# Kernel tuning notes

Measured on AMD Instinct MI355X. Metric: run time of the kernel, lower is better.

## Reference

```python
import jax, jax.numpy as jnp
import numpy as np

N, NFEAT, NHID, NCLASS = 10000, 512, 64, 10
ALPHA = 0.2


def setup_inputs() -> dict:
    key = jax.random.key(0)
    ks = jax.random.split(key, 8)
    x = jax.random.normal(ks[0], (N, NFEAT), dtype=jnp.float32)
    adj1 = jax.random.uniform(ks[1], (N, N), dtype=jnp.float32) / N  # row-normalized-ish
    adj2 = jax.random.uniform(ks[2], (N, N), dtype=jnp.float32) / N
    # GraphConvolution params (glorot-ish scale)
    W1 = jax.random.normal(ks[3], (NFEAT, NHID), dtype=jnp.float32) * (1.0 / np.sqrt(NFEAT))
    b1 = jnp.zeros((NHID,), dtype=jnp.float32)
    W2 = jax.random.normal(ks[4], (NFEAT, NHID), dtype=jnp.float32) * (1.0 / np.sqrt(NFEAT))
    b2 = jnp.zeros((NHID,), dtype=jnp.float32)
    attn_w = jax.random.normal(ks[5], (NHID, 1), dtype=jnp.float32) * (1.0 / np.sqrt(NHID))
    cluster = jax.random.normal(ks[6], (NCLASS, NHID), dtype=jnp.float32)
    return {"x": x, "adj1": adj1, "adj2": adj2, "W1": W1, "b1": b1,
            "W2": W2, "b2": b2, "attn_w": attn_w, "cluster": cluster}


def reference(x, adj1, adj2, W1, b1, W2, b2, attn_w, cluster):
    # Two GCN branches: output = adj @ (x @ W) + b
    emb1 = adj1 @ (x @ W1) + b1  # [N, H]
    emb2 = adj2 @ (x @ W2) + b2  # [N, H]
    z = jnp.stack([emb1, emb2], axis=1)            # [N, 2, H]
    # tiny 2-way attention fusion
    w = z @ attn_w                                  # [N, 2, 1]
    beta = jax.nn.softmax(w, axis=1)                # softmax over the 2 views
    emb = jnp.sum(beta * z, axis=1)                 # [N, H]
    # DEC cluster assignment (faithful to the original, including the
    # second power and the /2, which the row-normalization cancels)
    d2 = jnp.sum((emb[:, None, :] - cluster[None, :, :]) ** 2, axis=2)  # [N, K]
    q = 1.0 / (1.0 + d2 / ALPHA)
    q = q ** ((ALPHA + 1.0) / 2.0)
    q = q ** (ALPHA + 1.0) / 2.0
    q = q / jnp.sum(q, axis=1, keepdims=True)
    return emb, q
```

## Files before the change

kernel.cpp:

```cpp
#include <hip/hip_runtime.h>
#include <math.h>

#define NROWS 10000
#define FEAT  512
#define NHID  64
#define NCLS  10
#define YT_STRIDE 10240
#define KB_PAD 320
#define NSPLIT 8
#define CHUNK 40

typedef __attribute__((ext_vector_type(8))) short short8;
typedef __attribute__((ext_vector_type(4))) float f32x4;

__device__ __forceinline__ short f2bf(float f) {
  union { float f; unsigned u; } v; v.f = f;
  unsigned r = v.u + 0x7fffu + ((v.u >> 16) & 1u);
  return (short)(r >> 16);
}

__device__ __forceinline__ float wsum64(float v) {
#pragma unroll
  for (int off = 32; off > 0; off >>= 1) v += __shfl_xor(v, off, 64);
  return v;
}

__device__ __forceinline__ void gload16(const void* g, void* l) {
  __builtin_amdgcn_global_load_lds(
      (const __attribute__((address_space(1))) unsigned int*)g,
      (__attribute__((address_space(3))) unsigned int*)l, 16, 0, 0);
}

__global__ __launch_bounds__(256) void prep_w(const float* __restrict__ W1,
                                              const float* __restrict__ W2,
                                              unsigned short* __restrict__ Wt1,
                                              unsigned short* __restrict__ Wt2) {
  int i = blockIdx.x * 256 + threadIdx.x;
  if (i >= FEAT * NHID) return;
  int k = i >> 6, h = i & 63;
  Wt1[h * FEAT + k] = (unsigned short)f2bf(W1[i]);
  Wt2[h * FEAT + k] = (unsigned short)f2bf(W2[i]);
}

__global__ __launch_bounds__(256) void gemm_xw(const float* __restrict__ x,
                                               const unsigned short* __restrict__ Wt1,
                                               const unsigned short* __restrict__ Wt2,
                                               unsigned short* __restrict__ Yt1,
                                               unsigned short* __restrict__ Yt2) {
  const int lane = threadIdx.x & 63;
  const int wave = threadIdx.x >> 6;
  const int job = blockIdx.x * 4 + wave;
  if (job >= 1250) return;
  const int br = (job >= 625) ? 1 : 0;
  const int tile = job - 625 * br;
  const unsigned short* Wt = br ? Wt2 : Wt1;
  unsigned short* Yt       = br ? Yt2 : Yt1;
  const int rowbase = tile * 16;
  const int r16 = lane & 15, g = lane >> 4, ga = g * 8;

  const float* arow = x + (size_t)(rowbase + r16) * FEAT + ga;
  const unsigned short* bp = Wt + (size_t)r16 * FEAT + ga;

  f32x4 acc[4];
#pragma unroll
  for (int t = 0; t < 4; ++t) acc[t] = (f32x4){0.f, 0.f, 0.f, 0.f};

#pragma unroll
  for (int kb = 0; kb < FEAT / 32; ++kb) {
    const int k0 = kb * 32;
    const f32x4* ap = (const f32x4*)(arow + k0);
    f32x4 a0 = ap[0], a1 = ap[1];
    short8 af;
    af[0] = f2bf(a0[0]); af[1] = f2bf(a0[1]); af[2] = f2bf(a0[2]); af[3] = f2bf(a0[3]);
    af[4] = f2bf(a1[0]); af[5] = f2bf(a1[1]); af[6] = f2bf(a1[2]); af[7] = f2bf(a1[3]);
#pragma unroll
    for (int t = 0; t < 4; ++t) {
      short8 bf = *(const short8*)(bp + (size_t)t * 16 * FEAT + k0);
      acc[t] = __builtin_amdgcn_mfma_f32_16x16x32_bf16(af, bf, acc[t], 0, 0, 0);
    }
  }
#pragma unroll
  for (int t = 0; t < 4; ++t)
#pragma unroll
    for (int rr = 0; rr < 4; ++rr)
      Yt[(size_t)(t * 16 + r16) * YT_STRIDE + (rowbase + g * 4 + rr)] =
          (unsigned short)f2bf(acc[t][rr]);
}

__global__ __launch_bounds__(256, 3) void gemm_adj(const float* __restrict__ adj1,
                                                   const float* __restrict__ adj2,
                                                   const unsigned short* __restrict__ Yt1,
                                                   const unsigned short* __restrict__ Yt2,
                                                   float* __restrict__ Ep) {
  __shared__ __attribute__((aligned(16))) float          Asm[4][2048];
  __shared__ __attribute__((aligned(16))) unsigned short Bsm[4][2048];

  const int sp = blockIdx.y;
  const int br = blockIdx.z;
  const float* adj         = br ? adj2 : adj1;
  const unsigned short* Yt = br ? Yt2 : Yt1;
  float* E = Ep + (size_t)(br * NSPLIT + sp) * NROWS * NHID;
  const int kb0 = sp * CHUNK;
  const int blockrow = blockIdx.x * 64;

  const int lane = threadIdx.x & 63;
  const int wave = threadIdx.x >> 6;

  const int l8 = lane >> 3, v = lane & 7;
  const int arow0 = wave * 16 + l8;
  const int arow1 = wave * 16 + 8 + l8;
  const int g0 = (v >> 1) ^ (arow0 & 3), g1 = (v >> 1) ^ (arow1 & 3);
  const int akoff0 = g0 * 8 + (v & 1) * 4;
  const int akoff1 = g1 * 8 + (v & 1) * 4;
  const float* abase0 = adj + (size_t)min(blockrow + arow0, NROWS - 1) * NROWS;
  const float* abase1 = adj + (size_t)min(blockrow + arow1, NROWS - 1) * NROWS;
  const int adst0 = (wave * 2 + 0) * 256 + lane * 4;
  const int adst1 = (wave * 2 + 1) * 256 + lane * 4;
  const int bj = (lane & 3) ^ (l8 & 3);
  const unsigned short* bbase =
      Yt + (size_t)(wave * 16 + (lane >> 2)) * YT_STRIDE + bj * 8;
  const int bdst = wave * 512 + lane * 8;

  const int r16 = lane & 15, g = lane >> 4;
  const int ard  = (wave * 16 + r16) * 32 + ((g ^ (r16 & 3)) * 8);
  const int bsw  = (g ^ ((r16 >> 1) & 3)) * 8;
  const int brd0 = (0 * 16 + r16) * 32 + bsw;
  const int brd1 = (1 * 16 + r16) * 32 + bsw;
  const int brd2 = (2 * 16 + r16) * 32 + bsw;
  const int brd3 = (3 * 16 + r16) * 32 + bsw;

  f32x4 acc0 = (f32x4){0.f, 0.f, 0.f, 0.f};
  f32x4 acc1 = acc0, acc2 = acc0, acc3 = acc0;

#define STAGE(T) { const int k0s = (kb0 + (T)) * 32; const int sl = (T) & 3;      \
    gload16(abase0 + min(k0s + akoff0, NROWS - 4), &Asm[sl][adst0]);              \
    gload16(abase1 + min(k0s + akoff1, NROWS - 4), &Asm[sl][adst1]);              \
    gload16(bbase + k0s, &Bsm[sl][bdst]); }

#define RC(T) { const int sl = (T) & 3;                                           \
    const f32x4* ap = (const f32x4*)&Asm[sl][ard];                                \
    f32x4 a0 = ap[0], a1 = ap[1];                                                 \
    short8 bf0 = *(const short8*)&Bsm[sl][brd0];                                  \
    short8 bf1 = *(const short8*)&Bsm[sl][brd1];                                  \
    short8 bf2 = *(const short8*)&Bsm[sl][brd2];                                  \
    short8 bf3 = *(const short8*)&Bsm[sl][brd3];                                  \
    short8 af;                                                                    \
    af[0] = f2bf(a0[0]); af[1] = f2bf(a0[1]); af[2] = f2bf(a0[2]); af[3] = f2bf(a0[3]); \
    af[4] = f2bf(a1[0]); af[5] = f2bf(a1[1]); af[6] = f2bf(a1[2]); af[7] = f2bf(a1[3]); \
    acc0 = __builtin_amdgcn_mfma_f32_16x16x32_bf16(af, bf0, acc0, 0, 0, 0);       \
    acc1 = __builtin_amdgcn_mfma_f32_16x16x32_bf16(af, bf1, acc1, 0, 0, 0);       \
    acc2 = __builtin_amdgcn_mfma_f32_16x16x32_bf16(af, bf2, acc2, 0, 0, 0);       \
    acc3 = __builtin_amdgcn_mfma_f32_16x16x32_bf16(af, bf3, acc3, 0, 0, 0); }

  STAGE(0) STAGE(1) STAGE(2) STAGE(3)

#pragma unroll 4
  for (int t = 0; t < CHUNK - 3; ++t) {
    asm volatile("s_waitcnt vmcnt(9)" ::: "memory");
    __builtin_amdgcn_sched_barrier(0);
    __builtin_amdgcn_s_barrier();
    RC(t)
    __builtin_amdgcn_s_barrier();
    if (t < CHUNK - 4) STAGE(t + 4)
  }
  asm volatile("s_waitcnt vmcnt(6)" ::: "memory");
  __builtin_amdgcn_sched_barrier(0);
  __builtin_amdgcn_s_barrier();
  RC(CHUNK - 3)
  asm volatile("s_waitcnt vmcnt(3)" ::: "memory");
  __builtin_amdgcn_sched_barrier(0);
  __builtin_amdgcn_s_barrier();
  RC(CHUNK - 2)
  asm volatile("s_waitcnt vmcnt(0)" ::: "memory");
  __builtin_amdgcn_sched_barrier(0);
  __builtin_amdgcn_s_barrier();
  RC(CHUNK - 1)
#undef STAGE
#undef RC

#pragma unroll
  for (int rr = 0; rr < 4; ++rr) {
    const int grow = blockrow + wave * 16 + g * 4 + rr;
    if (grow < NROWS) {
      float* e = E + (size_t)grow * NHID + r16;
      e[0]  = acc0[rr];
      e[16] = acc1[rr];
      e[32] = acc2[rr];
      e[48] = acc3[rr];
    }
  }
}

__global__ __launch_bounds__(256) void gemm_adj_dyn(const float* __restrict__ adj1,
                                                    const float* __restrict__ adj2,
                                                    const unsigned short* __restrict__ Yt1,
                                                    const unsigned short* __restrict__ Yt2,
                                                    float* __restrict__ Ep,
                                                    int nsplit, int chunk) {
  const int sp = blockIdx.y;
  const int br = blockIdx.z;
  const float* adj          = br ? adj2 : adj1;
  const unsigned short* Yt  = br ? Yt2 : Yt1;
  float* E = Ep + (size_t)(br * nsplit + sp) * NROWS * NHID;

  const int kb_begin = sp * chunk;
  const int kb_end   = min(kb_begin + chunk, KB_PAD);

  const int lane = threadIdx.x & 63;
  const int wave = threadIdx.x >> 6;
  const int rowbase = blockIdx.x * 64 + wave * 16;
  if (rowbase >= NROWS) return;
  const int r = lane & 15;
  const int g = lane >> 4;
  const int ga = g * 8;

  const float* arow = adj + (size_t)(rowbase + r) * NROWS;
  const size_t boff = (size_t)r * YT_STRIDE + ga;

  f32x4 acc0 = (f32x4){0.f, 0.f, 0.f, 0.f};
  f32x4 acc1 = acc0, acc2 = acc0, acc3 = acc0;

#pragma unroll 4
  for (int kb = kb_begin; kb < kb_end; ++kb) {
    const int k0 = kb * 32;
    const int kc = min(k0 + ga, 9992);
    const f32x4* ap = (const f32x4*)(arow + kc);
    f32x4 a0 = ap[0], a1 = ap[1];
    short8 af;
    af[0] = f2bf(a0[0]); af[1] = f2bf(a0[1]); af[2] = f2bf(a0[2]); af[3] = f2bf(a0[3]);
    af[4] = f2bf(a1[0]); af[5] = f2bf(a1[1]); af[6] = f2bf(a1[2]); af[7] = f2bf(a1[3]);
    short8 bf0 = *(const short8*)(Yt + boff + k0);
    short8 bf1 = *(const short8*)(Yt + boff + 16 * YT_STRIDE + k0);
    short8 bf2 = *(const short8*)(Yt + boff + 32 * YT_STRIDE + k0);
    short8 bf3 = *(const short8*)(Yt + boff + 48 * YT_STRIDE + k0);
    acc0 = __builtin_amdgcn_mfma_f32_16x16x32_bf16(af, bf0, acc0, 0, 0, 0);
    acc1 = __builtin_amdgcn_mfma_f32_16x16x32_bf16(af, bf1, acc1, 0, 0, 0);
    acc2 = __builtin_amdgcn_mfma_f32_16x16x32_bf16(af, bf2, acc2, 0, 0, 0);
    acc3 = __builtin_amdgcn_mfma_f32_16x16x32_bf16(af, bf3, acc3, 0, 0, 0);
  }

  const size_t ebase = (size_t)(rowbase + g * 4) * NHID + r;
#pragma unroll
  for (int rr = 0; rr < 4; ++rr) {
    E[ebase + (size_t)rr * NHID +  0] = acc0[rr];
    E[ebase + (size_t)rr * NHID + 16] = acc1[rr];
    E[ebase + (size_t)rr * NHID + 32] = acc2[rr];
    E[ebase + (size_t)rr * NHID + 48] = acc3[rr];
  }
}

__global__ __launch_bounds__(256) void fuse(const float* __restrict__ Ep,
                                            int nsplit,
                                            const float* __restrict__ b1,
                                            const float* __restrict__ b2,
                                            const float* __restrict__ aw,
                                            const float* __restrict__ cl,
                                            float* __restrict__ out) {
  const int lane = threadIdx.x & 63;
  const int wave = threadIdx.x >> 6;
  const int row = blockIdx.x * 4 + wave;
  if (row >= NROWS) return;

  const size_t off = (size_t)row * NHID + lane;
  const size_t bstride = (size_t)nsplit * NROWS * NHID;
  float e1 = b1[lane], e2 = b2[lane];
  for (int s = 0; s < nsplit; ++s) {
    e1 += Ep[(size_t)s * NROWS * NHID + off];
    e2 += Ep[bstride + (size_t)s * NROWS * NHID + off];
  }

  float a = aw[lane];
  float w1 = wsum64(e1 * a);
  float w2 = wsum64(e2 * a);
  float m = fmaxf(w1, w2);
  float x1 = expf(w1 - m), x2 = expf(w2 - m);
  float inv = 1.0f / (x1 + x2);
  float emb = (x1 * e1 + x2 * e2) * inv;
  out[off] = emb;

  float myq = 0.f, qs = 0.f;
#pragma unroll
  for (int c = 0; c < NCLS; ++c) {
    float d = emb - cl[c * NHID + lane];
    float s = wsum64(d * d);
    float t = exp2f(-0.72f * log2f(fmaf(5.0f, s, 1.0f)));
    qs += t;
    if (lane == c) myq = t;
  }
  if (lane < NCLS) out[(size_t)NROWS * NHID + (size_t)row * NCLS + lane] = myq / qs;
}

extern "C" void kernel_launch(void* const* d_in, const int* in_sizes, int n_in,
                              void* d_out, int out_size, void* d_ws, size_t ws_size,
                              hipStream_t stream) {
  const float* x    = (const float*)d_in[0];
  const float* adj1 = (const float*)d_in[1];
  const float* adj2 = (const float*)d_in[2];
  const float* W1   = (const float*)d_in[3];
  const float* b1   = (const float*)d_in[4];
  const float* W2   = (const float*)d_in[5];
  const float* b2   = (const float*)d_in[6];
  const float* aw   = (const float*)d_in[7];
  const float* cl   = (const float*)d_in[8];
  float* out = (float*)d_out;

  char* ws = (char*)d_ws;
  unsigned short* Yt1 = (unsigned short*)(ws + 0);
  unsigned short* Yt2 = (unsigned short*)(ws + 1310720);
  unsigned short* Wt1 = (unsigned short*)(ws + 2621440);
  unsigned short* Wt2 = (unsigned short*)(ws + 2686976);
  float* Ep           = (float*)(ws + 2752512);

  const size_t fixed = 2752512;
  const size_t per_split = 2ull * NROWS * NHID * 4ull;
  const bool static_ok = ws_size >= fixed + (size_t)NSPLIT * per_split;

  hipMemsetAsync(Yt1, 0, 2 * 1310720, stream);
  prep_w<<<dim3(128), dim3(256), 0, stream>>>(W1, W2, Wt1, Wt2);
  gemm_xw<<<dim3(313), dim3(256), 0, stream>>>(x, Wt1, Wt2, Yt1, Yt2);

  if (static_ok) {
    gemm_adj<<<dim3(157, NSPLIT, 2), dim3(256), 0, stream>>>(adj1, adj2, Yt1, Yt2, Ep);
    fuse<<<dim3(2500), dim3(256), 0, stream>>>(Ep, NSPLIT, b1, b2, aw, cl, out);
  } else {
    int nsplit = 1;
    if (ws_size > fixed + per_split) {
      size_t s = (ws_size - fixed) / per_split;
      nsplit = (int)(s < 8 ? s : 8);
      if (nsplit < 1) nsplit = 1;
    }
    const int chunk = (KB_PAD + nsplit - 1) / nsplit;
    gemm_adj_dyn<<<dim3(157, nsplit, 2), dim3(256), 0, stream>>>(adj1, adj2, Yt1, Yt2,
                                                                 Ep, nsplit, chunk);
    fuse<<<dim3(2500), dim3(256), 0, stream>>>(Ep, nsplit, b1, b2, aw, cl, out);
  }
}
```

Measured before the change: 258.8 us.

## Retile adjacency GEMM with 32-row blocks, 256-wide K tiles and swizzled Yt

Reworks the adj@Y kernel to use 32x64 output tiles split across 4 waves (2x2), K tiles of 256 with double-buffered LDS staging, and 4 K-splits instead of 8. The Yt intermediate is written with an XOR swizzle on the row index so LDS reads of B avoid bank conflicts, and the fallback kernel is updated to match. Larger per-stage transfers aim to cut barrier and issue overhead and halve the split partials read by the fuse step. In exchange, the LDS footprint (~128KB) limits occupancy to one block per CU, and the A-tile rows are now loaded twice across blocks relative to the previous 64-row tiles.

```diff
diff --git a/kernel.cpp b/kernel.cpp
--- a/kernel.cpp
+++ b/kernel.cpp
@@ -7,8 +7,9 @@
 #define NCLS  10
 #define YT_STRIDE 10240
 #define KB_PAD 320
-#define NSPLIT 8
-#define CHUNK 40
+#define TK    256
+#define NSPLIT 4
+#define TILES_PER_SPLIT 10
 
 typedef __attribute__((ext_vector_type(8))) short short8;
 typedef __attribute__((ext_vector_type(4))) float f32x4;
@@ -79,114 +80,109 @@
       acc[t] = __builtin_amdgcn_mfma_f32_16x16x32_bf16(af, bf, acc[t], 0, 0, 0);
     }
   }
+  const int sw = (r16 & 7) << 3;
 #pragma unroll
   for (int t = 0; t < 4; ++t)
 #pragma unroll
-    for (int rr = 0; rr < 4; ++rr)
-      Yt[(size_t)(t * 16 + r16) * YT_STRIDE + (rowbase + g * 4 + rr)] =
-          (unsigned short)f2bf(acc[t][rr]);
-}
-
-__global__ __launch_bounds__(256, 3) void gemm_adj(const float* __restrict__ adj1,
+    for (int rr = 0; rr < 4; ++rr) {
+      const int col = t * 16 + r16;
+      const int row = rowbase + g * 4 + rr;
+      Yt[(size_t)col * YT_STRIDE + (row ^ sw)] = (unsigned short)f2bf(acc[t][rr]);
+    }
+}
+
+__global__ __launch_bounds__(256, 1) void gemm_adj(const float* __restrict__ adj1,
                                                    const float* __restrict__ adj2,
                                                    const unsigned short* __restrict__ Yt1,
                                                    const unsigned short* __restrict__ Yt2,
                                                    float* __restrict__ Ep) {
-  __shared__ __attribute__((aligned(16))) float          Asm[4][2048];
-  __shared__ __attribute__((aligned(16))) unsigned short Bsm[4][2048];
+  __shared__ __attribute__((aligned(16))) float          Asm[2][32 * 256];
+  __shared__ __attribute__((aligned(16))) unsigned short Bsm[2][64 * 256];
 
   const int sp = blockIdx.y;
   const int br = blockIdx.z;
   const float* adj         = br ? adj2 : adj1;
   const unsigned short* Yt = br ? Yt2 : Yt1;
   float* E = Ep + (size_t)(br * NSPLIT + sp) * NROWS * NHID;
-  const int kb0 = sp * CHUNK;
-  const int blockrow = blockIdx.x * 64;
+  const int k_base = sp * (TILES_PER_SPLIT * TK);
+  const int blockrow = blockIdx.x * 32;
 
   const int lane = threadIdx.x & 63;
   const int wave = threadIdx.x >> 6;
 
-  const int l8 = lane >> 3, v = lane & 7;
-  const int arow0 = wave * 16 + l8;
-  const int arow1 = wave * 16 + 8 + l8;
-  const int g0 = (v >> 1) ^ (arow0 & 3), g1 = (v >> 1) ^ (arow1 & 3);
-  const int akoff0 = g0 * 8 + (v & 1) * 4;
-  const int akoff1 = g1 * 8 + (v & 1) * 4;
-  const float* abase0 = adj + (size_t)min(blockrow + arow0, NROWS - 1) * NROWS;
-  const float* abase1 = adj + (size_t)min(blockrow + arow1, NROWS - 1) * NROWS;
-  const int adst0 = (wave * 2 + 0) * 256 + lane * 4;
-  const int adst1 = (wave * 2 + 1) * 256 + lane * 4;
-  const int bj = (lane & 3) ^ (l8 & 3);
-  const unsigned short* bbase =
-      Yt + (size_t)(wave * 16 + (lane >> 2)) * YT_STRIDE + bj * 8;
-  const int bdst = wave * 512 + lane * 8;
-
+  const int a_el = lane * 4;
+  const int b_cl = lane >> 5;
+  const int b_el = (lane & 31) * 8;
+
+  const int wr = wave >> 1, wc = wave & 1;
   const int r16 = lane & 15, g = lane >> 4;
-  const int ard  = (wave * 16 + r16) * 32 + ((g ^ (r16 & 3)) * 8);
-  const int bsw  = (g ^ ((r16 >> 1) & 3)) * 8;
-  const int brd0 = (0 * 16 + r16) * 32 + bsw;
-  const int brd1 = (1 * 16 + r16) * 32 + bsw;
-  const int brd2 = (2 * 16 + r16) * 32 + bsw;
-  const int brd3 = (3 * 16 + r16) * 32 + bsw;
-
-  f32x4 acc0 = (f32x4){0.f, 0.f, 0.f, 0.f};
-  f32x4 acc1 = acc0, acc2 = acc0, acc3 = acc0;
-
-#define STAGE(T) { const int k0s = (kb0 + (T)) * 32; const int sl = (T) & 3;      \
-    gload16(abase0 + min(k0s + akoff0, NROWS - 4), &Asm[sl][adst0]);              \
-    gload16(abase1 + min(k0s + akoff1, NROWS - 4), &Asm[sl][adst1]);              \
-    gload16(bbase + k0s, &Bsm[sl][bdst]); }
-
-#define RC(T) { const int sl = (T) & 3;                                           \
-    const f32x4* ap = (const f32x4*)&Asm[sl][ard];                                \
-    f32x4 a0 = ap[0], a1 = ap[1];                                                 \
-    short8 bf0 = *(const short8*)&Bsm[sl][brd0];                                  \
-    short8 bf1 = *(const short8*)&Bsm[sl][brd1];                                  \
-    short8 bf2 = *(const short8*)&Bsm[sl][brd2];                                  \
-    short8 bf3 = *(const short8*)&Bsm[sl][brd3];                                  \
-    short8 af;                                                                    \
-    af[0] = f2bf(a0[0]); af[1] = f2bf(a0[1]); af[2] = f2bf(a0[2]); af[3] = f2bf(a0[3]); \
-    af[4] = f2bf(a1[0]); af[5] = f2bf(a1[1]); af[6] = f2bf(a1[2]); af[7] = f2bf(a1[3]); \
-    acc0 = __builtin_amdgcn_mfma_f32_16x16x32_bf16(af, bf0, acc0, 0, 0, 0);       \
-    acc1 = __builtin_amdgcn_mfma_f32_16x16x32_bf16(af, bf1, acc1, 0, 0, 0);       \
-    acc2 = __builtin_amdgcn_mfma_f32_16x16x32_bf16(af, bf2, acc2, 0, 0, 0);       \
-    acc3 = __builtin_amdgcn_mfma_f32_16x16x32_bf16(af, bf3, acc3, 0, 0, 0); }
-
-  STAGE(0) STAGE(1) STAGE(2) STAGE(3)
-
-#pragma unroll 4
-  for (int t = 0; t < CHUNK - 3; ++t) {
-    asm volatile("s_waitcnt vmcnt(9)" ::: "memory");
+  const int swb = (r16 & 7) << 3;
+
+  f32x4 accL = (f32x4){0.f, 0.f, 0.f, 0.f};
+  f32x4 accH = accL;
+
+  auto STAGE = [&](int tt) {
+    const int k0 = k_base + tt * TK;
+    const int bufi = tt & 1;
+#pragma unroll
+    for (int j = 0; j < 8; ++j) {
+      const int gr = blockrow + wave * 8 + j;
+      const float* src = adj + (size_t)min(gr, NROWS - 1) * NROWS
+                             + min(k0 + a_el, NROWS - 4);
+      gload16(src, &Asm[bufi][(wave * 8 + j) * 256]);
+    }
+#pragma unroll
+    for (int j = 0; j < 8; ++j) {
+      const int c0 = wave * 16 + j * 2;
+      const unsigned short* src =
+          Yt + (size_t)(c0 + b_cl) * YT_STRIDE + (k0 + b_el);
+      gload16(src, &Bsm[bufi][c0 * 256]);
+    }
+  };
+
+  auto COMPUTE = [&](int tt) {
+    const int bufi = tt & 1;
+#pragma unroll
+    for (int s = 0; s < 8; ++s) {
+      const int kx = s * 32 + g * 8;
+      const float* ap = &Asm[bufi][(wr * 16 + r16) * 256 + kx];
+      f32x4 a0 = *(const f32x4*)ap;
+      f32x4 a1 = *(const f32x4*)(ap + 4);
+      const int colL = wc * 32 + r16;
+      short8 bL = *(const short8*)&Bsm[bufi][colL * 256 + (kx ^ swb)];
+      short8 bH = *(const short8*)&Bsm[bufi][(colL + 16) * 256 + (kx ^ swb)];
+      short8 af;
+      af[0] = f2bf(a0[0]); af[1] = f2bf(a0[1]); af[2] = f2bf(a0[2]); af[3] = f2bf(a0[3]);
+      af[4] = f2bf(a1[0]); af[5] = f2bf(a1[1]); af[6] = f2bf(a1[2]); af[7] = f2bf(a1[3]);
+      accL = __builtin_amdgcn_mfma_f32_16x16x32_bf16(af, bL, accL, 0, 0, 0);
+      accH = __builtin_amdgcn_mfma_f32_16x16x32_bf16(af, bH, accH, 0, 0, 0);
+    }
+  };
+
+  STAGE(0);
+#pragma unroll 2
+  for (int t = 0; t < TILES_PER_SPLIT - 1; ++t) {
+    STAGE(t + 1);
+    asm volatile("s_waitcnt vmcnt(16)" ::: "memory");
     __builtin_amdgcn_sched_barrier(0);
     __builtin_amdgcn_s_barrier();
-    RC(t)
+    __builtin_amdgcn_sched_barrier(0);
+    COMPUTE(t);
     __builtin_amdgcn_s_barrier();
-    if (t < CHUNK - 4) STAGE(t + 4)
-  }
-  asm volatile("s_waitcnt vmcnt(6)" ::: "memory");
-  __builtin_amdgcn_sched_barrier(0);
-  __builtin_amdgcn_s_barrier();
-  RC(CHUNK - 3)
-  asm volatile("s_waitcnt vmcnt(3)" ::: "memory");
-  __builtin_amdgcn_sched_barrier(0);
-  __builtin_amdgcn_s_barrier();
-  RC(CHUNK - 2)
+  }
   asm volatile("s_waitcnt vmcnt(0)" ::: "memory");
   __builtin_amdgcn_sched_barrier(0);
   __builtin_amdgcn_s_barrier();
-  RC(CHUNK - 1)
-#undef STAGE
-#undef RC
+  __builtin_amdgcn_sched_barrier(0);
+  COMPUTE(TILES_PER_SPLIT - 1);
 
 #pragma unroll
   for (int rr = 0; rr < 4; ++rr) {
-    const int grow = blockrow + wave * 16 + g * 4 + rr;
+    const int grow = blockrow + wr * 16 + g * 4 + rr;
     if (grow < NROWS) {
-      float* e = E + (size_t)grow * NHID + r16;
-      e[0]  = acc0[rr];
-      e[16] = acc1[rr];
-      e[32] = acc2[rr];
-      e[48] = acc3[rr];
+      float* e = E + (size_t)grow * NHID + wc * 32 + r16;
+      e[0]  = accL[rr];
+      e[16] = accH[rr];
     }
   }
 }
@@ -213,9 +209,9 @@
   const int r = lane & 15;
   const int g = lane >> 4;
   const int ga = g * 8;
+  const int sw = (r & 7) << 3;
 
   const float* arow = adj + (size_t)(rowbase + r) * NROWS;
-  const size_t boff = (size_t)r * YT_STRIDE + ga;
 
   f32x4 acc0 = (f32x4){0.f, 0.f, 0.f, 0.f};
   f32x4 acc1 = acc0, acc2 = acc0, acc3 = acc0;
@@ -224,15 +220,16 @@
   for (int kb = kb_begin; kb < kb_end; ++kb) {
     const int k0 = kb * 32;
     const int kc = min(k0 + ga, 9992);
+    const int ks = (k0 + ga) ^ sw;
     const f32x4* ap = (const f32x4*)(arow + kc);
     f32x4 a0 = ap[0], a1 = ap[1];
     short8 af;
     af[0] = f2bf(a0[0]); af[1] = f2bf(a0[1]); af[2] = f2bf(a0[2]); af[3] = f2bf(a0[3]);
     af[4] = f2bf(a1[0]); af[5] = f2bf(a1[1]); af[6] = f2bf(a1[2]); af[7] = f2bf(a1[3]);
-    short8 bf0 = *(const short8*)(Yt + boff + k0);
-    short8 bf1 = *(const short8*)(Yt + boff + 16 * YT_STRIDE + k0);
-    short8 bf2 = *(const short8*)(Yt + boff + 32 * YT_STRIDE + k0);
-    short8 bf3 = *(const short8*)(Yt + boff + 48 * YT_STRIDE + k0);
+    short8 bf0 = *(const short8*)(Yt + (size_t)(0 * 16 + r) * YT_STRIDE + ks);
+    short8 bf1 = *(const short8*)(Yt + (size_t)(1 * 16 + r) * YT_STRIDE + ks);
+    short8 bf2 = *(const short8*)(Yt + (size_t)(2 * 16 + r) * YT_STRIDE + ks);
+    short8 bf3 = *(const short8*)(Yt + (size_t)(3 * 16 + r) * YT_STRIDE + ks);
     acc0 = __builtin_amdgcn_mfma_f32_16x16x32_bf16(af, bf0, acc0, 0, 0, 0);
     acc1 = __builtin_amdgcn_mfma_f32_16x16x32_bf16(af, bf1, acc1, 0, 0, 0);
     acc2 = __builtin_amdgcn_mfma_f32_16x16x32_bf16(af, bf2, acc2, 0, 0, 0);
@@ -320,7 +317,7 @@
   gemm_xw<<<dim3(313), dim3(256), 0, stream>>>(x, Wt1, Wt2, Yt1, Yt2);
 
   if (static_ok) {
-    gemm_adj<<<dim3(157, NSPLIT, 2), dim3(256), 0, stream>>>(adj1, adj2, Yt1, Yt2, Ep);
+    gemm_adj<<<dim3(313, NSPLIT, 2), dim3(256), 0, stream>>>(adj1, adj2, Yt1, Yt2, Ep);
     fuse<<<dim3(2500), dim3(256), 0, stream>>>(Ep, NSPLIT, b1, b2, aw, cl, out);
   } else {
     int nsplit = 1;
```

New measurement: 321.0 us. +24.0%, slower.
